# Optimization experiments

Hardware: AMD Instinct MI355X
Metric: run time of the kernel (lower is better)

The kernel has to match this reference:

```python
import jax, jax.numpy as jnp
import numpy as np

B, T, D, H = 4, 4096, 2048, 128

def setup_inputs() -> dict:
    key = jax.random.key(0)
    k1, k2, k3, k4 = jax.random.split(key, 4)
    scale = 0.02
    return {
        "x": jax.random.normal(k1, (B, T, D), dtype=jnp.float32),
        "Wq": jax.random.normal(k2, (D, H), dtype=jnp.float32) * scale,
        "Wk": jax.random.normal(k3, (D, H), dtype=jnp.float32) * scale,
        "Wv": jax.random.normal(k4, (D, H), dtype=jnp.float32) * scale,
    }

def reference(x, Wq, Wk, Wv):
    # x: [B,T,D]; projections to [B,T,H]
    q = jnp.einsum('btd,dh->bth', x, Wq)
    k = jnp.einsum('btd,dh->bth', x, Wk)
    v = jnp.einsum('btd,dh->bth', x, Wv)
    scale = 1.0 / jnp.sqrt(jnp.asarray(q.shape[-1], q.dtype))
    scores = jnp.einsum('bth,bsh->bts', q, k) * scale  # [B,T,T]
    t = x.shape[1]
    causal = jnp.tril(jnp.ones((t, t), dtype=bool))
    scores = jnp.where(causal, scores, -jnp.inf)
    weights = jax.nn.softmax(scores, axis=-1)
    # dropout p=0.0 (eval) -> identity
    out = jnp.einsum('bts,bsh->bth', weights, v)
    return out
```

## Files before the change

kernel.cpp:

```cpp
#include <hip/hip_runtime.h>
#include <hip/hip_bf16.h>

#define Bq 4
#define Tq 4096
#define Dq 2048
#define Hq 128
#define Mq (Bq*Tq)
#define CHUNK 16

typedef __attribute__((ext_vector_type(8))) short bf16x8;
typedef __attribute__((ext_vector_type(4))) float f32x4;

static __device__ __forceinline__ short bfbits(float f) {
    union { __hip_bfloat16 h; short s; } u;
    u.h = __float2bfloat16(f);
    return u.s;
}
static __device__ __forceinline__ float bf2f(short s) {
    union { unsigned u; float f; } v;
    v.u = ((unsigned)(unsigned short)s) << 16;
    return v.f;
}
#define WAIT_LDS() __builtin_amdgcn_s_waitcnt(0xC07F)

static __device__ __forceinline__ void gload16(const void* g, void* l) {
    __builtin_amdgcn_global_load_lds(
        (const __attribute__((address_space(1))) unsigned int*)g,
        (__attribute__((address_space(3))) unsigned int*)l, 16, 0, 0);
}

__global__ __launch_bounds__(256, 1) void wt_kernel(
    const float* __restrict__ Wqp,
    const float* __restrict__ Wkp,
    const float* __restrict__ Wvp,
    short* __restrict__ wTg)
{
    __shared__ short trsp[128][136];
    const int kc = blockIdx.x;
    const int w  = blockIdx.y;
    const float* __restrict__ W = (w == 0) ? Wqp : (w == 1) ? Wkp : Wvp;
    const float scale = (w == 0) ? 0.08838834764831843f : 1.0f;
    const int t = threadIdx.x;

    #pragma unroll
    for (int i = 0; i < 16; i++) {
        int idx = t + i * 256;
        int r = idx >> 5, c4 = idx & 31;
        float4 f = *(const float4*)&W[(size_t)(kc * 128 + r) * Hq + c4 * 4];
        trsp[c4 * 4 + 0][r] = bfbits(f.x * scale);
        trsp[c4 * 4 + 1][r] = bfbits(f.y * scale);
        trsp[c4 * 4 + 2][r] = bfbits(f.z * scale);
        trsp[c4 * 4 + 3][r] = bfbits(f.w * scale);
    }
    __syncthreads();
    #pragma unroll
    for (int i = 0; i < 8; i++) {
        int idx = t + i * 256;
        int h = idx >> 4, c8 = idx & 15;
        *(bf16x8*)&wTg[((size_t)w * 128 + h) * Dq + kc * 128 + c8 * 8] =
            *(bf16x8*)&trsp[h][c8 * 8];
    }
}

__global__ __launch_bounds__(512, 2) void qkv_fused_kernel(
    const float* __restrict__ x,
    const short* __restrict__ wTg,
    short* __restrict__ qg,
    short* __restrict__ kg,
    short* __restrict__ vTt)
{
    __shared__ __attribute__((aligned(128))) char smem[114688];

    const int bid  = blockIdx.x;
    const int mi   = bid & 127;
    const int ni   = bid >> 7;
    const int m0   = mi * 128;
    const int n0   = ni * 192;

    const int t    = threadIdx.x;
    const int l    = t & 63;
    const int w    = t >> 6;
    const int l15  = l & 15;
    const int quad = l >> 4;
    const int wmi  = w & 3;
    const int wni  = w >> 2;
    const int swzA = l15 << 4;
    const int swzB = (l15 & 7) << 4;

    f32x4 o[2][6];
    #pragma unroll
    for (int mf = 0; mf < 2; mf++)
        #pragma unroll
        for (int j = 0; j < 6; j++) o[mf][j] = (f32x4){0.f, 0.f, 0.f, 0.f};

    const short* wsrc0 = wTg + (size_t)(n0 + 24 * w + (l >> 3)) * Dq
                             + (((l & 7) ^ (l >> 3)) << 3);

    #define ISSUE(it2, par)                                                      \
        do {                                                                     \
            char* wb_ = smem + (par) * 24576;                                    \
            _Pragma("unroll")                                                    \
            for (int j = 0; j < 3; j++)                                          \
                gload16(wsrc0 + (size_t)j * 8 * Dq + (it2) * 64,                 \
                        wb_ + (w * 3 + j) * 1024);                               \
            char* xb_ = smem + 49152 + (par) * 32768;                            \
            _Pragma("unroll")                                                    \
            for (int j = 0; j < 4; j++) {                                        \
                int row_ = 16 * w + 4 * j + (l >> 4);                            \
                int col_ = ((l & 15) ^ (4 * j + (l >> 4))) << 2;                 \
                gload16(x + (size_t)(m0 + row_) * Dq + (it2) * 64 + col_,        \
                        xb_ + (w * 4 + j) * 1024);                               \
            }                                                                    \
        } while (0)

    #define PHASE(par, kk)                                                       \
        do {                                                                     \
            const char* wb_ = smem + (par) * 24576;                              \
            const char* xb_ = smem + 49152 + (par) * 32768;                      \
            f32x4 f0[2], f1[2];                                                  \
            bf16x8 b[6];                                                         \
            const int kb = (kk) * 128 + quad * 32;                               \
            _Pragma("unroll")                                                    \
            for (int mf = 0; mf < 2; mf++) {                                     \
                const char* rp = xb_ + (wmi * 32 + mf * 16 + l15) * 256;         \
                f0[mf] = *(const f32x4*)(rp + (kb ^ swzA));                      \
                f1[mf] = *(const f32x4*)(rp + ((kb + 16) ^ swzA));               \
            }                                                                    \
            _Pragma("unroll")                                                    \
            for (int j = 0; j < 6; j++)                                          \
                b[j] = *(const bf16x8*)(wb_ + (wni * 96 + j * 16 + l15) * 128    \
                                            + (((kk) * 64 + quad * 16) ^ swzB)); \
            asm volatile("s_waitcnt lgkmcnt(0)" ::: "memory");                   \
            __builtin_amdgcn_sched_barrier(0);                                   \
            __builtin_amdgcn_s_setprio(1);                                       \
            _Pragma("unroll")                                                    \
            for (int mf = 0; mf < 2; mf++) {                                     \
                bf16x8 af;                                                       \
                af[0] = bfbits(f0[mf][0]); af[1] = bfbits(f0[mf][1]);            \
                af[2] = bfbits(f0[mf][2]); af[3] = bfbits(f0[mf][3]);            \
                af[4] = bfbits(f1[mf][0]); af[5] = bfbits(f1[mf][1]);            \
                af[6] = bfbits(f1[mf][2]); af[7] = bfbits(f1[mf][3]);            \
                _Pragma("unroll")                                                \
                for (int j = 0; j < 6; j++)                                      \
                    o[mf][j] = __builtin_amdgcn_mfma_f32_16x16x32_bf16(          \
                        af, b[j], o[mf][j], 0, 0, 0);                            \
            }                                                                    \
            __builtin_amdgcn_s_setprio(0);                                       \
        } while (0)

    ISSUE(0, 0);
    ISSUE(1, 1);
    asm volatile("s_waitcnt vmcnt(7)" ::: "memory");
    __builtin_amdgcn_sched_barrier(0);
    __builtin_amdgcn_s_barrier();

    #pragma unroll 1
    for (int it = 0; it < 32; ++it) {
        const int p = it & 1;
        PHASE(p, 0);
        PHASE(p, 1);
        __builtin_amdgcn_s_barrier();
        __builtin_amdgcn_sched_barrier(0);
        if (it < 30) {
            ISSUE(it + 2, p);
            asm volatile("s_waitcnt vmcnt(7)" ::: "memory");
        } else if (it == 30) {
            asm volatile("s_waitcnt vmcnt(0)" ::: "memory");
        }
        if (it < 31) {
            __builtin_amdgcn_sched_barrier(0);
            __builtin_amdgcn_s_barrier();
        }
    }

    #undef PHASE
    #undef ISSUE

    {
        short (*e)[200] = (short(*)[200])smem;
        #pragma unroll
        for (int mf = 0; mf < 2; mf++)
            #pragma unroll
            for (int j = 0; j < 6; j++) {
                int nloc = wni * 96 + j * 16;
                if (n0 + nloc < 256) {
                    #pragma unroll
                    for (int reg = 0; reg < 4; reg++)
                        e[wmi * 32 + mf * 16 + quad * 4 + reg][nloc + l15] =
                            bfbits(o[mf][j][reg]);
                }
            }
        __syncthreads();
        const int r  = t >> 2;
        const int u0 = (t & 3) * 6;
        #pragma unroll
        for (int i = 0; i < 6; i++) {
            int u  = u0 + i;
            int ng = n0 + u * 8;
            if (ng < 256) {
                bf16x8 val = *(bf16x8*)&e[r][u * 8];
                short* dst = (ng < 128) ? &qg[(size_t)(m0 + r) * Hq + ng]
                                        : &kg[(size_t)(m0 + r) * Hq + (ng - 128)];
                *(bf16x8*)dst = val;
            }
        }
    }
    if (ni == 1) {
        __syncthreads();
        short (*ev)[136] = (short(*)[136])(smem + 53248);
        #pragma unroll
        for (int mf = 0; mf < 2; mf++)
            #pragma unroll
            for (int j = 0; j < 6; j++) {
                int nloc = wni * 96 + j * 16;
                if (nloc >= 64) {
                    short4 pk;
                    pk.x = bfbits(o[mf][j][0]); pk.y = bfbits(o[mf][j][1]);
                    pk.z = bfbits(o[mf][j][2]); pk.w = bfbits(o[mf][j][3]);
                    *(short4*)&ev[(nloc - 64) + l15][wmi * 32 + mf * 16 + quad * 4] = pk;
                }
            }
        __syncthreads();
        const int bb  = m0 / Tq;
        const int jt0 = (m0 % Tq) >> 6;
        #pragma unroll
        for (int i = 0; i < 4; i++) {
            int idx = t + i * 512;
            int h = idx >> 4, u = idx & 15;
            int m = u * 8;
            int jt = jt0 + (m >> 6);
            *(bf16x8*)&vTt[(((size_t)bb * (Tq / 64) + jt) * 128 + h) * 64 + (m & 63)] =
                *(bf16x8*)&ev[h][m];
        }
    }
}

__global__ __launch_bounds__(256, 3) void attn_part_kernel(
    const short* __restrict__ qg, const short* __restrict__ kg,
    const short* __restrict__ vTt,
    short* __restrict__ Opart,
    float* __restrict__ lv)
{
    __shared__ short ks_s[64][136];
    __shared__ short vt_s[128][72];
    __shared__ short ps_s[64][72];

    const int qt = blockIdx.x;
    const int b  = blockIdx.y;
    const int c  = blockIdx.z;
    const int q0 = qt * 64;

    const int lo = c * CHUNK;
    const int hi = min(qt + 1, lo + CHUNK);
    if (lo >= hi) return;

    const int t    = threadIdx.x;
    const int lane = t & 63;
    const int qw   = t >> 6;
    const int l15  = lane & 15;
    const int quad = lane >> 4;

    bf16x8 qf[4];
    {
        const short* qsrc = qg + (size_t)(b * Tq + q0 + qw * 16 + l15) * Hq + quad * 8;
        #pragma unroll
        for (int kk = 0; kk < 4; kk++)
            qf[kk] = *(const bf16x8*)(qsrc + kk * 32);
    }

    float lsum[4] = {0.f, 0.f, 0.f, 0.f};
    f32x4 o[8];
    #pragma unroll
    for (int nf = 0; nf < 8; nf++) o[nf] = (f32x4){0.f, 0.f, 0.f, 0.f};

    bf16x8 kreg[4], vreg[4];
    {
        const size_t kbase = (size_t)(b * Tq + lo * 64) * Hq;
        const short* vsrc = vTt + (((size_t)b * (Tq / 64) + lo) * 128) * 64;
        #pragma unroll
        for (int i = 0; i < 4; i++) {
            int idx = t + i * 256;
            kreg[i] = *(const bf16x8*)&kg[kbase + (size_t)(idx >> 4) * Hq + (idx & 15) * 8];
            vreg[i] = *(const bf16x8*)&vsrc[idx * 8];
        }
        #pragma unroll
        for (int i = 0; i < 4; i++) {
            int idx = t + i * 256;
            *(bf16x8*)&ks_s[idx >> 4][(idx & 15) * 8] = kreg[i];
            *(bf16x8*)&vt_s[idx >> 3][(idx & 7) * 8]  = vreg[i];
        }
    }
    __syncthreads();

    for (int jt = lo; jt < hi; jt++) {
        if (jt + 1 < hi) {
            const size_t kbase = (size_t)(b * Tq + (jt + 1) * 64) * Hq;
            const short* vsrc = vTt + (((size_t)b * (Tq / 64) + jt + 1) * 128) * 64;
            #pragma unroll
            for (int i = 0; i < 4; i++) {
                int idx = t + i * 256;
                kreg[i] = *(const bf16x8*)&kg[kbase + (size_t)(idx >> 4) * Hq + (idx & 15) * 8];
                vreg[i] = *(const bf16x8*)&vsrc[idx * 8];
            }
        }

        f32x4 sacc[4];
        #pragma unroll
        for (int nf = 0; nf < 4; nf++) sacc[nf] = (f32x4){0.f, 0.f, 0.f, 0.f};
        #pragma unroll
        for (int kk = 0; kk < 4; kk++) {
            bf16x8 bk[4];
            #pragma unroll
            for (int nf = 0; nf < 4; nf++)
                bk[nf] = *(bf16x8*)&ks_s[nf * 16 + l15][kk * 32 + quad * 8];
            #pragma unroll
            for (int nf = 0; nf < 4; nf++)
                sacc[nf] = __builtin_amdgcn_mfma_f32_16x16x32_bf16(qf[kk], bk[nf], sacc[nf], 0, 0, 0);
        }

        const bool diag = (jt == qt);
        #pragma unroll
        for (int reg = 0; reg < 4; reg++) {
            const int rloc = qw * 16 + quad * 4 + reg;
            #pragma unroll
            for (int nf = 0; nf < 4; nf++) {
                float s = sacc[nf][reg];
                if (diag && (nf * 16 + l15 > rloc)) s = -1e30f;
                float p = __expf(s);
                lsum[reg] += p;
                ps_s[rloc][nf * 16 + l15] = bfbits(p);
            }
        }
        WAIT_LDS();

        #pragma unroll
        for (int ks2 = 0; ks2 < 2; ks2++) {
            bf16x8 ap = *(bf16x8*)&ps_s[qw * 16 + l15][ks2 * 32 + quad * 8];
            bf16x8 bv[8];
            #pragma unroll
            for (int nf = 0; nf < 8; nf++)
                bv[nf] = *(bf16x8*)&vt_s[nf * 16 + l15][ks2 * 32 + quad * 8];
            #pragma unroll
            for (int nf = 0; nf < 8; nf++)
                o[nf] = __builtin_amdgcn_mfma_f32_16x16x32_bf16(ap, bv[nf], o[nf], 0, 0, 0);
        }

        __syncthreads();
        if (jt + 1 < hi) {
            #pragma unroll
            for (int i = 0; i < 4; i++) {
                int idx = t + i * 256;
                *(bf16x8*)&ks_s[idx >> 4][(idx & 15) * 8] = kreg[i];
                *(bf16x8*)&vt_s[idx >> 3][(idx & 7) * 8]  = vreg[i];
            }
            __syncthreads();
        }
    }

    #pragma unroll
    for (int reg = 0; reg < 4; reg++) {
        #pragma unroll
        for (int mm = 8; mm >= 1; mm >>= 1)
            lsum[reg] += __shfl_xor(lsum[reg], mm, 16);
    }
    const size_t zoff = (size_t)c * Mq;
    if (l15 == 0) {
        #pragma unroll
        for (int reg = 0; reg < 4; reg++)
            lv[zoff + (size_t)b * Tq + q0 + qw * 16 + quad * 4 + reg] = lsum[reg];
    }

    __syncthreads();
    short (*epi)[136] = (short(*)[136])&ks_s[0][0];
    #pragma unroll
    for (int nf = 0; nf < 8; nf++)
        #pragma unroll
        for (int reg = 0; reg < 4; reg++)
            epi[qw * 16 + quad * 4 + reg][nf * 16 + l15] = bfbits(o[nf][reg]);
    __syncthreads();
    #pragma unroll
    for (int i = 0; i < 4; i++) {
        int idx = t + i * 256;
        int r = idx >> 4, cc = idx & 15;
        *(bf16x8*)&Opart[(zoff + (size_t)b * Tq + q0 + r) * Hq + cc * 8] =
            *(bf16x8*)&epi[r][cc * 8];
    }
}

__global__ __launch_bounds__(256, 4) void merge_kernel(
    const short* __restrict__ Opart, const float* __restrict__ lv,
    float* __restrict__ outg)
{
    const int t   = threadIdx.x;
    const int row = blockIdx.x * 16 + (t >> 4);
    const int cu  = t & 15;

    const int rl  = row & (Tq - 1);
    const int nch = (rl >> 10) + 1;

    float lsum = 0.f;
    float acc[8] = {};
    for (int cc = 0; cc < nch; cc++) {
        lsum += lv[(size_t)cc * Mq + row];
        bf16x8 oc = *(const bf16x8*)&Opart[((size_t)cc * Mq + row) * Hq + cu * 8];
        #pragma unroll
        for (int j = 0; j < 8; j++) acc[j] += bf2f(oc[j]);
    }
    float inv = 1.0f / lsum;

    float4 r0, r1;
    r0.x = acc[0] * inv; r0.y = acc[1] * inv; r0.z = acc[2] * inv; r0.w = acc[3] * inv;
    r1.x = acc[4] * inv; r1.y = acc[5] * inv; r1.z = acc[6] * inv; r1.w = acc[7] * inv;
    float* dst = &outg[(size_t)row * Hq + cu * 8];
    *(float4*)dst       = r0;
    *(float4*)(dst + 4) = r1;
}

extern "C" void kernel_launch(void* const* d_in, const int* in_sizes, int n_in,
                              void* d_out, int out_size, void* d_ws, size_t ws_size,
                              hipStream_t stream) {
    const float* x   = (const float*)d_in[0];
    const float* Wqp = (const float*)d_in[1];
    const float* Wkp = (const float*)d_in[2];
    const float* Wvp = (const float*)d_in[3];
    float* out = (float*)d_out;

    short* qg    = (short*)d_ws;
    short* kg    = qg  + (size_t)Mq * Hq;
    short* vTt   = kg  + (size_t)Mq * Hq;
    short* Opart = vTt + (size_t)Mq * Hq;
    short* wTg   = Opart;
    float* lv    = (float*)(Opart + (size_t)4 * Mq * Hq);

    wt_kernel<<<dim3(16, 3), dim3(256), 0, stream>>>(Wqp, Wkp, Wvp, wTg);
    qkv_fused_kernel<<<dim3(256), dim3(512), 0, stream>>>(x, wTg, qg, kg, vTt);
    attn_part_kernel<<<dim3(Tq / 64, Bq, 4), dim3(256), 0, stream>>>(qg, kg, vTt, Opart, lv);
    merge_kernel<<<dim3(Mq / 16), dim3(256), 0, stream>>>(Opart, lv, out);
}
```

Measured before the change: 265.1 us.

## Halve QKV projection M-tile to 64 rows, doubling grid and occupancy

```diff
diff --git a/kernel.cpp b/kernel.cpp
--- a/kernel.cpp
+++ b/kernel.cpp
@@ -62,19 +62,19 @@
     }
 }
 
-__global__ __launch_bounds__(512, 2) void qkv_fused_kernel(
+__global__ __launch_bounds__(512, 4) void qkv_fused_kernel(
     const float* __restrict__ x,
     const short* __restrict__ wTg,
     short* __restrict__ qg,
     short* __restrict__ kg,
     short* __restrict__ vTt)
 {
-    __shared__ __attribute__((aligned(128))) char smem[114688];
+    __shared__ __attribute__((aligned(128))) char smem[81920];
 
     const int bid  = blockIdx.x;
-    const int mi   = bid & 127;
-    const int ni   = bid >> 7;
-    const int m0   = mi * 128;
+    const int mi   = bid & 255;
+    const int ni   = bid >> 8;
+    const int m0   = mi * 64;
     const int n0   = ni * 192;
 
     const int t    = threadIdx.x;
@@ -82,43 +82,44 @@
     const int w    = t >> 6;
     const int l15  = l & 15;
     const int quad = l >> 4;
-    const int wmi  = w & 3;
-    const int wni  = w >> 2;
+    const int wmi  = w & 1;
+    const int wni  = w >> 1;
     const int swzA = l15 << 4;
     const int swzB = (l15 & 7) << 4;
 
-    f32x4 o[2][6];
+    f32x4 o[2][3];
     #pragma unroll
     for (int mf = 0; mf < 2; mf++)
         #pragma unroll
-        for (int j = 0; j < 6; j++) o[mf][j] = (f32x4){0.f, 0.f, 0.f, 0.f};
+        for (int j = 0; j < 3; j++) o[mf][j] = (f32x4){0.f, 0.f, 0.f, 0.f};
 
     const short* wsrc0 = wTg + (size_t)(n0 + 24 * w + (l >> 3)) * Dq
                              + (((l & 7) ^ (l >> 3)) << 3);
 
     #define ISSUE(it2, par)                                                      \
         do {                                                                     \
-            char* wb_ = smem + (par) * 24576;                                    \
+            char* xb_ = smem + (par) * 40960;                                    \
+            char* wb_ = xb_ + 16384;                                             \
+            _Pragma("unroll")                                                    \
+            for (int j = 0; j < 2; j++) {                                        \
+                int c_   = w * 2 + j;                                            \
+                int row_ = 4 * c_ + (l >> 4);                                    \
+                int col_ = ((l & 15) ^ (4 * (c_ & 3) + (l >> 4))) << 2;          \
+                gload16(x + (size_t)(m0 + row_) * Dq + (it2) * 64 + col_,        \
+                        xb_ + c_ * 1024);                                        \
+            }                                                                    \
             _Pragma("unroll")                                                    \
             for (int j = 0; j < 3; j++)                                          \
                 gload16(wsrc0 + (size_t)j * 8 * Dq + (it2) * 64,                 \
                         wb_ + (w * 3 + j) * 1024);                               \
-            char* xb_ = smem + 49152 + (par) * 32768;                            \
-            _Pragma("unroll")                                                    \
-            for (int j = 0; j < 4; j++) {                                        \
-                int row_ = 16 * w + 4 * j + (l >> 4);                            \
-                int col_ = ((l & 15) ^ (4 * j + (l >> 4))) << 2;                 \
-                gload16(x + (size_t)(m0 + row_) * Dq + (it2) * 64 + col_,        \
-                        xb_ + (w * 4 + j) * 1024);                               \
-            }                                                                    \
         } while (0)
 
     #define PHASE(par, kk)                                                       \
         do {                                                                     \
-            const char* wb_ = smem + (par) * 24576;                              \
-            const char* xb_ = smem + 49152 + (par) * 32768;                      \
+            const char* xb_ = smem + (par) * 40960;                              \
+            const char* wb_ = xb_ + 16384;                                       \
             f32x4 f0[2], f1[2];                                                  \
-            bf16x8 b[6];                                                         \
+            bf16x8 b[3];                                                         \
             const int kb = (kk) * 128 + quad * 32;                               \
             _Pragma("unroll")                                                    \
             for (int mf = 0; mf < 2; mf++) {                                     \
@@ -127,8 +128,8 @@
                 f1[mf] = *(const f32x4*)(rp + ((kb + 16) ^ swzA));               \
             }                                                                    \
             _Pragma("unroll")                                                    \
-            for (int j = 0; j < 6; j++)                                          \
-                b[j] = *(const bf16x8*)(wb_ + (wni * 96 + j * 16 + l15) * 128    \
+            for (int j = 0; j < 3; j++)                                          \
+                b[j] = *(const bf16x8*)(wb_ + (wni * 48 + j * 16 + l15) * 128    \
                                             + (((kk) * 64 + quad * 16) ^ swzB)); \
             asm volatile("s_waitcnt lgkmcnt(0)" ::: "memory");                   \
             __builtin_amdgcn_sched_barrier(0);                                   \
@@ -141,7 +142,7 @@
                 af[4] = bfbits(f1[mf][0]); af[5] = bfbits(f1[mf][1]);            \
                 af[6] = bfbits(f1[mf][2]); af[7] = bfbits(f1[mf][3]);            \
                 _Pragma("unroll")                                                \
-                for (int j = 0; j < 6; j++)                                      \
+                for (int j = 0; j < 3; j++)                                      \
                     o[mf][j] = __builtin_amdgcn_mfma_f32_16x16x32_bf16(          \
                         af, b[j], o[mf][j], 0, 0, 0);                            \
             }                                                                    \
@@ -150,27 +151,19 @@
 
     ISSUE(0, 0);
     ISSUE(1, 1);
-    asm volatile("s_waitcnt vmcnt(7)" ::: "memory");
-    __builtin_amdgcn_sched_barrier(0);
-    __builtin_amdgcn_s_barrier();
 
     #pragma unroll 1
     for (int it = 0; it < 32; ++it) {
         const int p = it & 1;
+        if (it < 31) asm volatile("s_waitcnt vmcnt(5)" ::: "memory");
+        else         asm volatile("s_waitcnt vmcnt(0)" ::: "memory");
+        __builtin_amdgcn_sched_barrier(0);
+        __builtin_amdgcn_s_barrier();
         PHASE(p, 0);
         PHASE(p, 1);
         __builtin_amdgcn_s_barrier();
         __builtin_amdgcn_sched_barrier(0);
-        if (it < 30) {
-            ISSUE(it + 2, p);
-            asm volatile("s_waitcnt vmcnt(7)" ::: "memory");
-        } else if (it == 30) {
-            asm volatile("s_waitcnt vmcnt(0)" ::: "memory");
-        }
-        if (it < 31) {
-            __builtin_amdgcn_sched_barrier(0);
-            __builtin_amdgcn_s_barrier();
-        }
+        if (it < 30) ISSUE(it + 2, p);
     }
 
     #undef PHASE
@@ -181,8 +174,8 @@
         #pragma unroll
         for (int mf = 0; mf < 2; mf++)
             #pragma unroll
-            for (int j = 0; j < 6; j++) {
-                int nloc = wni * 96 + j * 16;
+            for (int j = 0; j < 3; j++) {
+                int nloc = wni * 48 + j * 16;
                 if (n0 + nloc < 256) {
                     #pragma unroll
                     for (int reg = 0; reg < 4; reg++)
@@ -191,10 +184,10 @@
                 }
             }
         __syncthreads();
-        const int r  = t >> 2;
-        const int u0 = (t & 3) * 6;
-        #pragma unroll
-        for (int i = 0; i < 6; i++) {
+        const int r  = t >> 3;
+        const int u0 = (t & 7) * 3;
+        #pragma unroll
+        for (int i = 0; i < 3; i++) {
             int u  = u0 + i;
             int ng = n0 + u * 8;
             if (ng < 256) {
@@ -207,12 +200,12 @@
     }
     if (ni == 1) {
         __syncthreads();
-        short (*ev)[136] = (short(*)[136])(smem + 53248);
+        short (*ev)[72] = (short(*)[72])smem;
         #pragma unroll
         for (int mf = 0; mf < 2; mf++)
             #pragma unroll
-            for (int j = 0; j < 6; j++) {
-                int nloc = wni * 96 + j * 16;
+            for (int j = 0; j < 3; j++) {
+                int nloc = wni * 48 + j * 16;
                 if (nloc >= 64) {
                     short4 pk;
                     pk.x = bfbits(o[mf][j][0]); pk.y = bfbits(o[mf][j][1]);
@@ -221,16 +214,14 @@
                 }
             }
         __syncthreads();
-        const int bb  = m0 / Tq;
-        const int jt0 = (m0 % Tq) >> 6;
-        #pragma unroll
-        for (int i = 0; i < 4; i++) {
+        const int bb = m0 / Tq;
+        const int jt = (m0 % Tq) >> 6;
+        #pragma unroll
+        for (int i = 0; i < 2; i++) {
             int idx = t + i * 512;
-            int h = idx >> 4, u = idx & 15;
-            int m = u * 8;
-            int jt = jt0 + (m >> 6);
-            *(bf16x8*)&vTt[(((size_t)bb * (Tq / 64) + jt) * 128 + h) * 64 + (m & 63)] =
-                *(bf16x8*)&ev[h][m];
+            int h = idx >> 3, u = idx & 7;
+            *(bf16x8*)&vTt[(((size_t)bb * (Tq / 64) + jt) * 128 + h) * 64 + u * 8] =
+                *(bf16x8*)&ev[h][u * 8];
         }
     }
 }
@@ -433,7 +424,7 @@
     float* lv    = (float*)(Opart + (size_t)4 * Mq * Hq);
 
     wt_kernel<<<dim3(16, 3), dim3(256), 0, stream>>>(Wqp, Wkp, Wvp, wTg);
-    qkv_fused_kernel<<<dim3(256), dim3(512), 0, stream>>>(x, wTg, qg, kg, vTt);
+    qkv_fused_kernel<<<dim3(512), dim3(512), 0, stream>>>(x, wTg, qg, kg, vTt);
     attn_part_kernel<<<dim3(Tq / 64, Bq, 4), dim3(256), 0, stream>>>(qg, kg, vTt, Opart, lv);
     merge_kernel<<<dim3(Mq / 16), dim3(256), 0, stream>>>(Opart, lv, out);
 }
```

Result: slower. 276.5 us (+4.3%).
